# Kernel optimization log

Measured on AMD Instinct MI355X. Metric: run time of the kernel, lower is better.

Reference implementation:

```python
import jax, jax.numpy as jnp
import numpy as np

N, E = 50000, 800000
IN, HID, OUT = 128, 128, 64
H, ED = 4, 3
D = HID // H  # per-head dim = 32


def _w(key, shape):
    fan_in = shape[-1]
    return jax.random.normal(key, shape, dtype=jnp.float32) / np.sqrt(fan_in)


def setup_inputs() -> dict:
    key = jax.random.key(0)
    ks = jax.random.split(key, 32)
    inp = {
        "x": jax.random.normal(ks[0], (N, IN), dtype=jnp.float32),
        "edge_index": jax.random.randint(ks[1], (2, E), 0, N, dtype=jnp.int32),
        "edge_attr": jax.random.normal(ks[2], (E, ED), dtype=jnp.float32),
        # layer 1 TransformerConv (bias=False)
        "Wq1": _w(ks[3], (HID, IN)), "Wk1": _w(ks[4], (HID, IN)),
        "Wv1": _w(ks[5], (HID, IN)), "We1": _w(ks[6], (HID, ED)),
        "Ws1": _w(ks[7], (HID, IN)),
        # layer 1 MLP [HID,HID,HID]
        "M1a": _w(ks[8], (HID, HID)), "b1a": jnp.zeros((HID,), jnp.float32),
        "M1b": _w(ks[9], (HID, HID)), "b1b": jnp.zeros((HID,), jnp.float32),
        # layer 2 TransformerConv
        "Wq2": _w(ks[10], (HID, HID)), "Wk2": _w(ks[11], (HID, HID)),
        "Wv2": _w(ks[12], (HID, HID)), "We2": _w(ks[13], (HID, ED)),
        "Ws2": _w(ks[14], (HID, HID)),
        # layer 2 MLP
        "M2a": _w(ks[15], (HID, HID)), "b2a": jnp.zeros((HID,), jnp.float32),
        "M2b": _w(ks[16], (HID, HID)), "b2b": jnp.zeros((HID,), jnp.float32),
        # final MLP [HID,HID,OUT], plain_last=False
        "Wf1": _w(ks[17], (HID, HID)), "bf1": jnp.zeros((HID,), jnp.float32),
        "Wf2": _w(ks[18], (OUT, HID)), "bf2": jnp.zeros((OUT,), jnp.float32),
    }
    return inp


def _gelu(x):
    return jax.nn.gelu(x, approximate=True)


def _transformer_conv(x, src, dst, edge_attr, Wq, Wk, Wv, We, Ws, n_nodes):
    # PyG TransformerConv: x_j = x[src] (message source), x_i = x[dst] (target)
    q = (x @ Wq.T).reshape(n_nodes, H, D)
    e = (edge_attr @ We.T).reshape(-1, H, D)              # [E,H,D]
    k = (x @ Wk.T).reshape(n_nodes, H, D)[src] + e        # [E,H,D]
    v = (x @ Wv.T).reshape(n_nodes, H, D)[src] + e        # [E,H,D]
    alpha = jnp.einsum("ehd,ehd->eh", q[dst], k) / jnp.float32(np.sqrt(D))
    # segment softmax over incoming edges of each target node
    m = jax.ops.segment_max(alpha, dst, num_segments=n_nodes)  # [N,H]
    m = jnp.where(jnp.isfinite(m), m, 0.0)
    p = jnp.exp(alpha - m[dst])
    s = jax.ops.segment_sum(p, dst, num_segments=n_nodes)      # [N,H]
    a = p / jnp.maximum(s[dst], 1e-16)                         # [E,H]
    out = jax.ops.segment_sum(a[:, :, None] * v, dst, num_segments=n_nodes)
    out = out.reshape(n_nodes, H * D)
    # root_weight=True (default): skip connection through lin_skip (no bias)
    return out + x @ Ws.T


def _mlp2(x, Wa, ba, Wb, bb):
    # PyG MLP with plain_last=False: act after every linear, norm=None
    h = _gelu(x @ Wa.T + ba)
    return _gelu(h @ Wb.T + bb)


def reference(x, edge_index, edge_attr,
              Wq1, Wk1, Wv1, We1, Ws1, M1a, b1a, M1b, b1b,
              Wq2, Wk2, Wv2, We2, Ws2, M2a, b2a, M2b, b2b,
              Wf1, bf1, Wf2, bf2):
    n_nodes = x.shape[0]
    src, dst = edge_index[0], edge_index[1]
    h = _transformer_conv(x, src, dst, edge_attr, Wq1, Wk1, Wv1, We1, Ws1, n_nodes)
    h = h + _mlp2(h, M1a, b1a, M1b, b1b)
    h = _transformer_conv(h, src, dst, edge_attr, Wq2, Wk2, Wv2, We2, Ws2, n_nodes)
    h = h + _mlp2(h, M2a, b2a, M2b, b2b)
    return _mlp2(h, Wf1, bf1, Wf2, bf2)
```

## Files before the change

### kernel.cpp

```cpp
#include <hip/hip_runtime.h>
#include <hip/hip_bf16.h>
#include <math.h>

#define NN 50000
#define NE 800000
#define NPAD 50048
#define NB_SCAN 196

typedef unsigned short u16;
typedef unsigned int u32;
typedef __attribute__((ext_vector_type(8))) short short8;
typedef __attribute__((ext_vector_type(4))) float float4v;

__device__ __forceinline__ float us2f(u16 u) { return __uint_as_float(((unsigned)u) << 16); }
__device__ __forceinline__ float blo(u32 u) { return __uint_as_float(u << 16); }
__device__ __forceinline__ float bhi(u32 u) { return __uint_as_float(u & 0xffff0000u); }
__device__ __forceinline__ u16 f2us(float f) {
    unsigned x = __float_as_uint(f);
    return (u16)((x + 0x7FFFu + ((x >> 16) & 1u)) >> 16);
}
__device__ __forceinline__ float gelu_f(float x) {
    float p = x * x;
    float t = x * fmaf(p, 0.0713548162726f, 1.5957691216057308f);
    float e = __expf(-t);
    return x * __builtin_amdgcn_rcpf(1.0f + e);
}
__device__ __forceinline__ void lds_fence() {
    asm volatile("s_waitcnt lgkmcnt(0)" ::: "memory");
}

__device__ __forceinline__ float4v mfma4p(const u16* __restrict__ WP, int tile, int l,
                                          short8 a0, short8 a1, short8 a2, short8 a3) {
    const short8* wp = (const short8*)WP + (size_t)tile * 256 + l;
    short8 b0 = wp[0], b1 = wp[64], b2 = wp[128], b3 = wp[192];
    float4v acc = {0.f, 0.f, 0.f, 0.f};
    acc = __builtin_amdgcn_mfma_f32_16x16x32_bf16(a0, b0, acc, 0, 0, 0);
    acc = __builtin_amdgcn_mfma_f32_16x16x32_bf16(a1, b1, acc, 0, 0, 0);
    acc = __builtin_amdgcn_mfma_f32_16x16x32_bf16(a2, b2, acc, 0, 0, 0);
    acc = __builtin_amdgcn_mfma_f32_16x16x32_bf16(a3, b3, acc, 0, 0, 0);
    return acc;
}


__global__ void k_hist(const int* __restrict__ dstv, int* __restrict__ deg) {
    int e = blockIdx.x * blockDim.x + threadIdx.x;
    if (e < NE) atomicAdd(&deg[dstv[e]], 1);
}

__global__ __launch_bounds__(256) void k_scan1(const int* __restrict__ deg,
                                               int* __restrict__ rowstart,
                                               int* __restrict__ bsum) {
    __shared__ int wtot[4];
    int i = blockIdx.x * 256 + threadIdx.x;
    int lane = threadIdx.x & 63, w = threadIdx.x >> 6;
    int v = (i < NN) ? deg[i] : 0;
    int incl = v;
#pragma unroll
    for (int d = 1; d < 64; d <<= 1) {
        int tv = __shfl_up(incl, d);
        if (lane >= d) incl += tv;
    }
    if (lane == 63) wtot[w] = incl;
    __syncthreads();
    if (threadIdx.x == 0) {
        int s = 0;
#pragma unroll
        for (int j = 0; j < 4; ++j) { int t = wtot[j]; wtot[j] = s; s += t; }
        bsum[blockIdx.x] = s;
    }
    __syncthreads();
    if (i < NN) rowstart[i] = incl - v + wtot[w];
}

__global__ __launch_bounds__(256) void k_scan2(int* __restrict__ bsum) {
    __shared__ int wtot[4];
    int t = threadIdx.x;
    int lane = t & 63, w = t >> 6;
    int v = (t < NB_SCAN) ? bsum[t] : 0;
    int incl = v;
#pragma unroll
    for (int d = 1; d < 64; d <<= 1) {
        int tv = __shfl_up(incl, d);
        if (lane >= d) incl += tv;
    }
    if (lane == 63) wtot[w] = incl;
    __syncthreads();
    if (t == 0) {
        int s = 0;
#pragma unroll
        for (int j = 0; j < 4; ++j) { int tt = wtot[j]; wtot[j] = s; s += tt; }
    }
    __syncthreads();
    if (t < NB_SCAN) bsum[t] = incl - v + wtot[w];
}

__global__ void k_scan3(const int* __restrict__ bsum, int* __restrict__ rowstart,
                        int* __restrict__ cursor) {
    int i = blockIdx.x * 256 + threadIdx.x;
    if (i < NN) {
        int v = rowstart[i] + bsum[blockIdx.x];
        rowstart[i] = v;
        cursor[i] = v;
    }
    if (i == 0) rowstart[NN] = NE;
}

__global__ void k_scatter(const int* __restrict__ srcv, const int* __restrict__ dstv,
                          const float* __restrict__ eattr, int* __restrict__ cursor,
                          int4* __restrict__ rec) {
    int e = blockIdx.x * blockDim.x + threadIdx.x;
    if (e >= NE) return;
    int dst = dstv[e];
    int pos = atomicAdd(&cursor[dst], 1);
    int4 r;
    r.x = srcv[e];
    r.y = __float_as_int(eattr[e * 3 + 0]);
    r.z = __float_as_int(eattr[e * 3 + 1]);
    r.w = __float_as_int(eattr[e * 3 + 2]);
    rec[pos] = r;
}


struct CvtEnt { const float* s; u16* d; int n; float sc; };
struct CvtTab { CvtEnt e[14]; };
__global__ void k_cvt_w(CvtTab tab) {
    CvtEnt E = tab.e[blockIdx.x >> 3];
    int chunk = blockIdx.x & 7;
    int per = E.n >> 3;
    int lo = chunk * per, hi = lo + per;
    for (int o = lo + threadIdx.x; o < hi; o += blockDim.x) {
        int tile = o >> 11;
        int q = (o >> 9) & 3;
        int l = (o >> 3) & 63;
        int j = o & 7;
        int row = tile * 16 + (l & 15);
        int col = q * 32 + (l >> 4) * 8 + j;
        E.d[o] = f2us(E.s[row * 128 + col] * E.sc);
    }
}


__device__ __forceinline__ void stage_plain(u16* buf, int kb, int m, int tt, float4v acc) {
#pragma unroll
    for (int r = 0; r < 4; ++r) buf[(kb * 4 + r) * 136 + tt * 16 + m] = f2us(acc[r]);
}
__device__ __forceinline__ void store128(const u16* buf, u16* dst, int r0w, int coff, int l) {
#pragma unroll
    for (int it = 0; it < 4; ++it) {
        int j = it * 64 + l;
        int row = j >> 4, col = (j & 15) * 8;
        *(uint4*)(dst + (size_t)(r0w + row) * 512 + coff + col) = *(const uint4*)&buf[row * 136 + col];
    }
}
__device__ __forceinline__ void read_frags(const u16* buf, int m, int kb,
                                           short8& f0, short8& f1, short8& f2, short8& f3) {
    const u16* p = buf + m * 136 + kb * 8;
    f0 = *(const short8*)(p);
    f1 = *(const short8*)(p + 32);
    f2 = *(const short8*)(p + 64);
    f3 = *(const short8*)(p + 96);
}


__global__ __launch_bounds__(256, 4) void k_qkvs1(const float* __restrict__ Ain,
                                                  const u16* __restrict__ W,
                                                  u16* __restrict__ QKVS) {
    __shared__ u16 tile[4][16 * 136];
    int tid = threadIdx.x;
    int l = tid & 63, w = tid >> 6, m = l & 15, kb = l >> 4;
    int r0w = blockIdx.x * 64 + w * 16;
    u16* my = tile[w];

    short8 a0, a1, a2, a3;
    {
        const float* ap = Ain + (size_t)(r0w + m) * 128;
        bool ok = (r0w + m) < NN;
        short8* dsts[4] = {&a0, &a1, &a2, &a3};
#pragma unroll
        for (int i = 0; i < 4; ++i) {
            short8 r;
            if (ok) {
                const float* p = ap + (kb + i * 4) * 8;
                float4 f0 = *(const float4*)p;
                float4 f1 = *(const float4*)(p + 4);
                r[0]=(short)f2us(f0.x); r[1]=(short)f2us(f0.y); r[2]=(short)f2us(f0.z); r[3]=(short)f2us(f0.w);
                r[4]=(short)f2us(f1.x); r[5]=(short)f2us(f1.y); r[6]=(short)f2us(f1.z); r[7]=(short)f2us(f1.w);
            } else {
#pragma unroll
                for (int j = 0; j < 8; ++j) r[j] = 0;
            }
            *dsts[i] = r;
        }
    }

#pragma unroll
    for (int tt = 0; tt < 8; ++tt) stage_plain(my, kb, m, tt, mfma4p(W, tt, l, a0, a1, a2, a3));
    lds_fence();
    store128(my, QKVS, r0w, 0, l);
    lds_fence();
#pragma unroll
    for (int tt = 0; tt < 4; ++tt) {
        float4v acc = mfma4p(W, 8 + tt, l, a0, a1, a2, a3);
        int c = tt * 32 + 8 * (m >> 2) + (m & 3);
#pragma unroll
        for (int r = 0; r < 4; ++r) my[(kb * 4 + r) * 136 + c] = f2us(acc[r]);
    }
#pragma unroll
    for (int tt = 0; tt < 4; ++tt) {
        float4v acc = mfma4p(W, 16 + tt, l, a0, a1, a2, a3);
        int c = tt * 32 + 8 * (m >> 2) + (m & 3) + 4;
#pragma unroll
        for (int r = 0; r < 4; ++r) my[(kb * 4 + r) * 136 + c] = f2us(acc[r]);
    }
    lds_fence();
    store128(my, QKVS, r0w, 128, l);
    lds_fence();
#pragma unroll
    for (int tt = 0; tt < 4; ++tt) {
        float4v acc = mfma4p(W, 12 + tt, l, a0, a1, a2, a3);
        int c = tt * 32 + 8 * (m >> 2) + (m & 3);
#pragma unroll
        for (int r = 0; r < 4; ++r) my[(kb * 4 + r) * 136 + c] = f2us(acc[r]);
    }
#pragma unroll
    for (int tt = 0; tt < 4; ++tt) {
        float4v acc = mfma4p(W, 20 + tt, l, a0, a1, a2, a3);
        int c = tt * 32 + 8 * (m >> 2) + (m & 3) + 4;
#pragma unroll
        for (int r = 0; r < 4; ++r) my[(kb * 4 + r) * 136 + c] = f2us(acc[r]);
    }
    lds_fence();
    store128(my, QKVS, r0w, 256, l);
    lds_fence();
#pragma unroll
    for (int tt = 0; tt < 8; ++tt) stage_plain(my, kb, m, tt, mfma4p(W, 24 + tt, l, a0, a1, a2, a3));
    lds_fence();
    store128(my, QKVS, r0w, 384, l);
}


__global__ __launch_bounds__(256, 4) void k_mlp_qkvs(const u16* __restrict__ Ain,
                                                     const u16* __restrict__ Wm,
                                                     const float* __restrict__ bias1,
                                                     const float* __restrict__ bias2,
                                                     const u16* __restrict__ Wq,
                                                     u16* __restrict__ QKVS) {
    __shared__ u16 shb[4][16 * 136];
    __shared__ u16 t1b[4][16 * 136];
    int tid = threadIdx.x;
    int l = tid & 63, w = tid >> 6, m = l & 15, kb = l >> 4;
    int r0w = blockIdx.x * 64 + w * 16;
    u16* sh = shb[w];
    u16* t1 = t1b[w];

    const short8* arow = (const short8*)(Ain + (size_t)(r0w + m) * 128);
    short8 a0 = arow[kb], a1 = arow[kb + 4], a2 = arow[kb + 8], a3 = arow[kb + 12];
    {
        u16* p = sh + m * 136 + kb * 8;
        *(short8*)(p) = a0;
        *(short8*)(p + 32) = a1;
        *(short8*)(p + 64) = a2;
        *(short8*)(p + 96) = a3;
    }
#pragma unroll
    for (int tt = 0; tt < 8; ++tt) {
        float4v acc = mfma4p(Wm, tt, l, a0, a1, a2, a3);
        float bv = bias1[tt * 16 + m];
#pragma unroll
        for (int r = 0; r < 4; ++r)
            t1[(kb * 4 + r) * 136 + tt * 16 + m] = f2us(gelu_f(acc[r] + bv));
    }
    lds_fence();
    short8 c0, c1, c2, c3;
    read_frags(t1, m, kb, c0, c1, c2, c3);
#pragma unroll
    for (int tt = 0; tt < 8; ++tt) {
        float4v acc = mfma4p(Wm + 16384, tt, l, c0, c1, c2, c3);
        float bv = bias2[tt * 16 + m];
#pragma unroll
        for (int r = 0; r < 4; ++r) {
            int idx = (kb * 4 + r) * 136 + tt * 16 + m;
            sh[idx] = f2us(gelu_f(acc[r] + bv) + us2f(sh[idx]));
        }
    }
    lds_fence();
    short8 h0, h1, h2, h3;
    read_frags(sh, m, kb, h0, h1, h2, h3);

#pragma unroll
    for (int tt = 0; tt < 8; ++tt) stage_plain(t1, kb, m, tt, mfma4p(Wq, tt, l, h0, h1, h2, h3));
    lds_fence();
    store128(t1, QKVS, r0w, 0, l);
    lds_fence();
#pragma unroll
    for (int tt = 0; tt < 4; ++tt) {
        float4v acc = mfma4p(Wq, 8 + tt, l, h0, h1, h2, h3);
        int c = tt * 32 + 8 * (m >> 2) + (m & 3);
#pragma unroll
        for (int r = 0; r < 4; ++r) t1[(kb * 4 + r) * 136 + c] = f2us(acc[r]);
    }
#pragma unroll
    for (int tt = 0; tt < 4; ++tt) {
        float4v acc = mfma4p(Wq, 16 + tt, l, h0, h1, h2, h3);
        int c = tt * 32 + 8 * (m >> 2) + (m & 3) + 4;
#pragma unroll
        for (int r = 0; r < 4; ++r) t1[(kb * 4 + r) * 136 + c] = f2us(acc[r]);
    }
    lds_fence();
    store128(t1, QKVS, r0w, 128, l);
    lds_fence();
#pragma unroll
    for (int tt = 0; tt < 4; ++tt) {
        float4v acc = mfma4p(Wq, 12 + tt, l, h0, h1, h2, h3);
        int c = tt * 32 + 8 * (m >> 2) + (m & 3);
#pragma unroll
        for (int r = 0; r < 4; ++r) t1[(kb * 4 + r) * 136 + c] = f2us(acc[r]);
    }
#pragma unroll
    for (int tt = 0; tt < 4; ++tt) {
        float4v acc = mfma4p(Wq, 20 + tt, l, h0, h1, h2, h3);
        int c = tt * 32 + 8 * (m >> 2) + (m & 3) + 4;
#pragma unroll
        for (int r = 0; r < 4; ++r) t1[(kb * 4 + r) * 136 + c] = f2us(acc[r]);
    }
    lds_fence();
    store128(t1, QKVS, r0w, 256, l);
    lds_fence();
#pragma unroll
    for (int tt = 0; tt < 8; ++tt) stage_plain(t1, kb, m, tt, mfma4p(Wq, 24 + tt, l, h0, h1, h2, h3));
    lds_fence();
    store128(t1, QKVS, r0w, 384, l);
}


__global__ __launch_bounds__(256, 4) void k_mlp_final(const u16* __restrict__ Ain,
                                                      const u16* __restrict__ Wm,
                                                      const float* __restrict__ bias1,
                                                      const float* __restrict__ bias2,
                                                      const u16* __restrict__ Wf,
                                                      const float* __restrict__ bf1,
                                                      const float* __restrict__ bf2,
                                                      float* __restrict__ outp) {
    __shared__ u16 shb[4][16 * 136];
    __shared__ u16 t1b[4][16 * 136];
    int tid = threadIdx.x;
    int l = tid & 63, w = tid >> 6, m = l & 15, kb = l >> 4;
    int r0w = blockIdx.x * 64 + w * 16;
    u16* sh = shb[w];
    u16* t1 = t1b[w];

    const short8* arow = (const short8*)(Ain + (size_t)(r0w + m) * 128);
    short8 a0 = arow[kb], a1 = arow[kb + 4], a2 = arow[kb + 8], a3 = arow[kb + 12];
    {
        u16* p = sh + m * 136 + kb * 8;
        *(short8*)(p) = a0;
        *(short8*)(p + 32) = a1;
        *(short8*)(p + 64) = a2;
        *(short8*)(p + 96) = a3;
    }
#pragma unroll
    for (int tt = 0; tt < 8; ++tt) {
        float4v acc = mfma4p(Wm, tt, l, a0, a1, a2, a3);
        float bv = bias1[tt * 16 + m];
#pragma unroll
        for (int r = 0; r < 4; ++r)
            t1[(kb * 4 + r) * 136 + tt * 16 + m] = f2us(gelu_f(acc[r] + bv));
    }
    lds_fence();
    short8 c0, c1, c2, c3;
    read_frags(t1, m, kb, c0, c1, c2, c3);
#pragma unroll
    for (int tt = 0; tt < 8; ++tt) {
        float4v acc = mfma4p(Wm + 16384, tt, l, c0, c1, c2, c3);
        float bv = bias2[tt * 16 + m];
#pragma unroll
        for (int r = 0; r < 4; ++r) {
            int idx = (kb * 4 + r) * 136 + tt * 16 + m;
            sh[idx] = f2us(gelu_f(acc[r] + bv) + us2f(sh[idx]));
        }
    }
    lds_fence();
    short8 h0, h1, h2, h3;
    read_frags(sh, m, kb, h0, h1, h2, h3);
#pragma unroll
    for (int tt = 0; tt < 8; ++tt) {
        float4v acc = mfma4p(Wf, tt, l, h0, h1, h2, h3);
        float bv = bf1[tt * 16 + m];
#pragma unroll
        for (int r = 0; r < 4; ++r)
            t1[(kb * 4 + r) * 136 + tt * 16 + m] = f2us(gelu_f(acc[r] + bv));
    }
    lds_fence();
    short8 f0, f1, f2, f3;
    read_frags(t1, m, kb, f0, f1, f2, f3);
    lds_fence();
#pragma unroll
    for (int tt = 0; tt < 4; ++tt) {
        float4v acc = mfma4p(Wf + 16384, tt, l, f0, f1, f2, f3);
        float bv = bf2[tt * 16 + m];
#pragma unroll
        for (int r = 0; r < 4; ++r)
            t1[(kb * 4 + r) * 136 + tt * 16 + m] = f2us(gelu_f(acc[r] + bv));
    }
    lds_fence();
#pragma unroll
    for (int it = 0; it < 2; ++it) {
        int j = it * 64 + l;
        int row = j >> 3, col = (j & 7) * 8;
        int grow = r0w + row;
        if (grow < NN) {
            uint4 pk = *(const uint4*)&t1[row * 136 + col];
            const u16* pv = (const u16*)&pk;
            float* po = outp + (size_t)grow * 64 + col;
            float4 o0 = {us2f(pv[0]), us2f(pv[1]), us2f(pv[2]), us2f(pv[3])};
            float4 o1 = {us2f(pv[4]), us2f(pv[5]), us2f(pv[6]), us2f(pv[7])};
            *(float4*)po = o0;
            *(float4*)(po + 4) = o1;
        }
    }
}


__global__ __launch_bounds__(256, 6) void k_conv(const int* __restrict__ rowstart,
                                                 const int4* __restrict__ rec,
                                                 const u16* __restrict__ qkvs,
                                                 const float* __restrict__ We,
                                                 u16* __restrict__ out) {
    int n = blockIdx.x * 4 + (threadIdx.x >> 6);
    int l = threadIdx.x & 63;
    int half = l >> 5;
    int li = l & 31;
    int c0 = (li >> 3) * 32 + (li & 7) * 4;
    const u16* qrow = qkvs + (size_t)n * 512;
    uint2 qu = *(const uint2*)(qrow + c0);
    uint2 su = *(const uint2*)(qrow + 384 + c0);
    float q0 = blo(qu.x), q1 = bhi(qu.x), q2 = blo(qu.y), q3 = bhi(qu.y);
    float g0, g1, g2;
    {
        const float* wp = We + c0 * 3;
        g0 = fmaf(q3, wp[9],  fmaf(q2, wp[6], fmaf(q1, wp[3], q0 * wp[0])));
        g1 = fmaf(q3, wp[10], fmaf(q2, wp[7], fmaf(q1, wp[4], q0 * wp[1])));
        g2 = fmaf(q3, wp[11], fmaf(q2, wp[8], fmaf(q1, wp[5], q0 * wp[2])));
#pragma unroll
        for (int d = 1; d <= 4; d <<= 1) {
            g0 += __shfl_xor(g0, d);
            g1 += __shfl_xor(g1, d);
            g2 += __shfl_xor(g2, d);
        }
    }
    int e0 = rowstart[n], e1 = rowstart[n + 1];
    int cnt = e1 - e0;
    float ss = 0.f, o0 = 0.f, o1 = 0.f, o2 = 0.f, o3 = 0.f, S0 = 0.f, S1 = 0.f, S2 = 0.f;
    int kvoff = 128 + li * 8;

    auto edge = [&](int4 r, uint4 kv) {
        float part = fmaf(q3, bhi(kv.y), fmaf(q2, blo(kv.y), fmaf(q1, bhi(kv.x), q0 * blo(kv.x))));
        part += __shfl_xor(part, 1);
        part += __shfl_xor(part, 2);
        part += __shfl_xor(part, 4);
        float ea0 = __int_as_float(r.y), ea1 = __int_as_float(r.z), ea2 = __int_as_float(r.w);
        float alpha = fmaf(ea2, g2, fmaf(ea1, g1, fmaf(ea0, g0, part)));
        float p = __expf(fminf(alpha, 80.f));
        o0 = fmaf(p, blo(kv.z), o0);
        o1 = fmaf(p, bhi(kv.z), o1);
        o2 = fmaf(p, blo(kv.w), o2);
        o3 = fmaf(p, bhi(kv.w), o3);
        ss += p;
        S0 = fmaf(p, ea0, S0);
        S1 = fmaf(p, ea1, S1);
        S2 = fmaf(p, ea2, S2);
    };

    int Kh = (cnt - half + 1) >> 1;
    int e = e0 + half;
    int k = 0;
    for (; k + 4 <= Kh; k += 4, e += 8) {
        int4 r0 = rec[e], r1 = rec[e + 2], r2 = rec[e + 4], r3 = rec[e + 6];
        uint4 k0 = *(const uint4*)(qkvs + (u32)(r0.x * 512 + kvoff));
        uint4 k1 = *(const uint4*)(qkvs + (u32)(r1.x * 512 + kvoff));
        uint4 k2 = *(const uint4*)(qkvs + (u32)(r2.x * 512 + kvoff));
        uint4 k3 = *(const uint4*)(qkvs + (u32)(r3.x * 512 + kvoff));
        edge(r0, k0);
        edge(r1, k1);
        edge(r2, k2);
        edge(r3, k3);
    }
    if (k + 2 <= Kh) {
        int4 r0 = rec[e], r1 = rec[e + 2];
        uint4 k0 = *(const uint4*)(qkvs + (u32)(r0.x * 512 + kvoff));
        uint4 k1 = *(const uint4*)(qkvs + (u32)(r1.x * 512 + kvoff));
        edge(r0, k0);
        edge(r1, k1);
        k += 2;
        e += 4;
    }
    if (k < Kh) {
        int4 r0 = rec[e];
        uint4 k0 = *(const uint4*)(qkvs + (u32)(r0.x * 512 + kvoff));
        edge(r0, k0);
    }

    o0 += __shfl_xor(o0, 32);
    o1 += __shfl_xor(o1, 32);
    o2 += __shfl_xor(o2, 32);
    o3 += __shfl_xor(o3, 32);
    ss += __shfl_xor(ss, 32);
    S0 += __shfl_xor(S0, 32);
    S1 += __shfl_xor(S1, 32);
    S2 += __shfl_xor(S2, 32);
    if (half == 0) {
        float inv = __builtin_amdgcn_rcpf(fmaxf(ss, 1e-16f));
        const float* wp = We + c0 * 3;
        o0 = fmaf(wp[2],  S2, fmaf(wp[1],  S1, fmaf(wp[0], S0, o0)));
        o1 = fmaf(wp[5],  S2, fmaf(wp[4],  S1, fmaf(wp[3], S0, o1)));
        o2 = fmaf(wp[8],  S2, fmaf(wp[7],  S1, fmaf(wp[6], S0, o2)));
        o3 = fmaf(wp[11], S2, fmaf(wp[10], S1, fmaf(wp[9], S0, o3)));
        float r0v = fmaf(o0, inv, blo(su.x));
        float r1v = fmaf(o1, inv, bhi(su.x));
        float r2v = fmaf(o2, inv, blo(su.y));
        float r3v = fmaf(o3, inv, bhi(su.y));
        uint2 ou;
        ou.x = (u32)f2us(r0v) | ((u32)f2us(r1v) << 16);
        ou.y = (u32)f2us(r2v) | ((u32)f2us(r3v) << 16);
        *(uint2*)(out + (size_t)n * 128 + c0) = ou;
    }
}


extern "C" void kernel_launch(void* const* d_in, const int* in_sizes, int n_in,
                              void* d_out, int out_size, void* d_ws, size_t ws_size,
                              hipStream_t stream) {
    const float* x = (const float*)d_in[0];
    const int* ei = (const int*)d_in[1];
    const float* eattr = (const float*)d_in[2];
    const float* Wq1 = (const float*)d_in[3];
    const float* Wk1 = (const float*)d_in[4];
    const float* Wv1 = (const float*)d_in[5];
    const float* We1 = (const float*)d_in[6];
    const float* Ws1 = (const float*)d_in[7];
    const float* M1a = (const float*)d_in[8];
    const float* b1a = (const float*)d_in[9];
    const float* M1b = (const float*)d_in[10];
    const float* b1b = (const float*)d_in[11];
    const float* Wq2 = (const float*)d_in[12];
    const float* Wk2 = (const float*)d_in[13];
    const float* Wv2 = (const float*)d_in[14];
    const float* We2 = (const float*)d_in[15];
    const float* Ws2 = (const float*)d_in[16];
    const float* M2a = (const float*)d_in[17];
    const float* b2a = (const float*)d_in[18];
    const float* M2b = (const float*)d_in[19];
    const float* b2b = (const float*)d_in[20];
    const float* Wf1 = (const float*)d_in[21];
    const float* bf1 = (const float*)d_in[22];
    const float* Wf2 = (const float*)d_in[23];
    const float* bf2 = (const float*)d_in[24];

    char* ws = (char*)d_ws;
    size_t off = 0;
    auto alloc = [&](size_t bytes) -> void* {
        void* p = ws + off;
        off = (off + bytes + 255) & ~(size_t)255;
        return p;
    };
    int* deg = (int*)alloc((size_t)NN * 4);
    int* rowstart = (int*)alloc((size_t)(NN + 1) * 4);
    int* cursor = (int*)alloc((size_t)NN * 4);
    int* bsum = (int*)alloc((size_t)NB_SCAN * 4);
    int4* rec = (int4*)alloc((size_t)NE * 16);
    u16* QKVS = (u16*)alloc((size_t)NPAD * 512 * 2);
    u16* Ha = (u16*)alloc((size_t)NPAD * 128 * 2);
    u16* WB[14];
    const int wsz[14] = {16384, 16384, 16384, 16384, 16384, 16384, 16384,
                         16384, 16384, 16384, 16384, 16384, 16384, 8192};
    for (int i = 0; i < 14; ++i) WB[i] = (u16*)alloc((size_t)wsz[i] * 2);

    const int* srcv = ei;
    const int* dstv = ei + NE;

    hipMemsetAsync(deg, 0, (size_t)NN * 4, stream);
    k_hist<<<(NE + 255) / 256, 256, 0, stream>>>(dstv, deg);
    k_scan1<<<NB_SCAN, 256, 0, stream>>>(deg, rowstart, bsum);
    k_scan2<<<1, 256, 0, stream>>>(bsum);
    k_scan3<<<NB_SCAN, 256, 0, stream>>>(bsum, rowstart, cursor);
    k_scatter<<<(NE + 255) / 256, 256, 0, stream>>>(srcv, dstv, eattr, cursor, rec);

    CvtTab tab;
    const float* wsrc[14] = {Wq1, Wk1, Wv1, Ws1, Wq2, Wk2, Wv2, Ws2,
                             M1a, M1b, M2a, M2b, Wf1, Wf2};
    const float SC = 0.17677669529663687f;
    for (int i = 0; i < 14; ++i) {
        tab.e[i].s = wsrc[i];
        tab.e[i].d = WB[i];
        tab.e[i].n = wsz[i];
        tab.e[i].sc = (i == 0 || i == 4) ? SC : 1.0f;
    }
    k_cvt_w<<<112, 256, 0, stream>>>(tab);

    dim3 blk(256);
    dim3 grd(NPAD / 64);
    dim3 gconv(NN / 4);

    k_qkvs1<<<grd, blk, 0, stream>>>(x, WB[0], QKVS);
    k_conv<<<gconv, blk, 0, stream>>>(rowstart, rec, QKVS, We1, Ha);
    k_mlp_qkvs<<<grd, blk, 0, stream>>>(Ha, WB[8], b1a, b1b, WB[4], QKVS);
    k_conv<<<gconv, blk, 0, stream>>>(rowstart, rec, QKVS, We2, Ha);
    k_mlp_final<<<grd, blk, 0, stream>>>(Ha, WB[10], b2a, b2b, WB[12], bf1, bf2, (float*)d_out);
}
```

Measured before the change: 407.8 us.

## Quantize gathered K/V to int8 with per-row-head scales for edge conv

Result: no change. 406.4 us (-0.3%).

```diff
diff --git a/kernel.cpp b/kernel.cpp
--- a/kernel.cpp
+++ b/kernel.cpp
@@ -9,6 +9,7 @@
 
 typedef unsigned short u16;
 typedef unsigned int u32;
+typedef unsigned char u8;
 typedef __attribute__((ext_vector_type(8))) short short8;
 typedef __attribute__((ext_vector_type(4))) float float4v;
 
@@ -28,6 +29,20 @@
 __device__ __forceinline__ void lds_fence() {
     asm volatile("s_waitcnt lgkmcnt(0)" ::: "memory");
 }
+
+#if __has_builtin(__builtin_amdgcn_sdot4)
+__device__ __forceinline__ int dot4i8(int a, int b) {
+    return __builtin_amdgcn_sdot4(a, b, 0, false);
+}
+#else
+__device__ __forceinline__ int dot4i8(int a, int b) {
+    int r = ((a << 24) >> 24) * ((b << 24) >> 24);
+    r += ((a << 16) >> 24) * ((b << 16) >> 24);
+    r += ((a << 8) >> 24) * ((b << 8) >> 24);
+    r += (a >> 24) * (b >> 24);
+    return r;
+}
+#endif
 
 __device__ __forceinline__ float4v mfma4p(const u16* __restrict__ WP, int tile, int l,
                                           short8 a0, short8 a1, short8 a2, short8 a3) {
@@ -144,12 +159,49 @@
 #pragma unroll
     for (int r = 0; r < 4; ++r) buf[(kb * 4 + r) * 136 + tt * 16 + m] = f2us(acc[r]);
 }
-__device__ __forceinline__ void store128(const u16* buf, u16* dst, int r0w, int coff, int l) {
+__device__ __forceinline__ void store_qs(const u16* buf, u16* dst, int r0w, int coff, int l) {
 #pragma unroll
     for (int it = 0; it < 4; ++it) {
         int j = it * 64 + l;
         int row = j >> 4, col = (j & 15) * 8;
-        *(uint4*)(dst + (size_t)(r0w + row) * 512 + coff + col) = *(const uint4*)&buf[row * 136 + col];
+        *(uint4*)(dst + (size_t)(r0w + row) * 256 + coff + col) = *(const uint4*)&buf[row * 136 + col];
+    }
+}
+__device__ __forceinline__ void kv_scales(const u16* buf, float* sclw, float* __restrict__ SCL,
+                                          int r0w, int halfsel, int l) {
+    int rr = l & 15;
+    int hl = (l >> 4) & 1;
+    int kind = l >> 5;
+    const u16* base = buf + rr * 136 + hl * 64 + kind * 4;
+    unsigned mx = 0;
+#pragma unroll
+    for (int p = 0; p < 8; ++p) {
+        uint2 w = *(const uint2*)(base + p * 8);
+        unsigned a = w.x & 0x7fff7fffu, b = w.y & 0x7fff7fffu;
+        unsigned m1 = max(a & 0xffffu, a >> 16);
+        unsigned m2 = max(b & 0xffffu, b >> 16);
+        mx = max(mx, max(m1, m2));
+    }
+    float ma = fmaxf(us2f((u16)mx), 1e-20f);
+    float inv = 127.0f * __builtin_amdgcn_rcpf(ma);
+    sclw[rr * 4 + kind * 2 + hl] = inv;
+    SCL[(size_t)(r0w + rr) * 8 + (hl + halfsel * 2) * 2 + kind] = ma * (1.0f / 127.0f);
+}
+__device__ __forceinline__ void kv_to_i8(const u16* buf, const float* sclw,
+                                         u8* __restrict__ kvq, int r0w, int halfoff, int l) {
+    int ch = l & 31;
+    int rsel = l >> 5;
+#pragma unroll
+    for (int it = 0; it < 8; ++it) {
+        int rr = it * 2 + rsel;
+        uint2 w = *(const uint2*)&buf[rr * 136 + ch * 4];
+        float inv = sclw[rr * 4 + (ch & 1) * 2 + (ch >> 4)];
+        int i0 = __float2int_rn(blo(w.x) * inv);
+        int i1 = __float2int_rn(bhi(w.x) * inv);
+        int i2 = __float2int_rn(blo(w.y) * inv);
+        int i3 = __float2int_rn(bhi(w.y) * inv);
+        unsigned pk = (i0 & 255) | ((i1 & 255) << 8) | ((i2 & 255) << 16) | ((unsigned)(i3 & 255) << 24);
+        *(unsigned*)(kvq + (size_t)(r0w + rr) * 256 + halfoff + ch * 4) = pk;
     }
 }
 __device__ __forceinline__ void read_frags(const u16* buf, int m, int kb,
@@ -164,12 +216,16 @@
 
 __global__ __launch_bounds__(256, 4) void k_qkvs1(const float* __restrict__ Ain,
                                                   const u16* __restrict__ W,
-                                                  u16* __restrict__ QKVS) {
+                                                  u16* __restrict__ QS,
+                                                  u8* __restrict__ KVQ,
+                                                  float* __restrict__ SCL) {
     __shared__ u16 tile[4][16 * 136];
+    __shared__ float scl[4][64];
     int tid = threadIdx.x;
     int l = tid & 63, w = tid >> 6, m = l & 15, kb = l >> 4;
     int r0w = blockIdx.x * 64 + w * 16;
     u16* my = tile[w];
+    float* sw = scl[w];
 
     short8 a0, a1, a2, a3;
     {
@@ -196,7 +252,7 @@
 #pragma unroll
     for (int tt = 0; tt < 8; ++tt) stage_plain(my, kb, m, tt, mfma4p(W, tt, l, a0, a1, a2, a3));
     lds_fence();
-    store128(my, QKVS, r0w, 0, l);
+    store_qs(my, QS, r0w, 0, l);
     lds_fence();
 #pragma unroll
     for (int tt = 0; tt < 4; ++tt) {
@@ -213,7 +269,9 @@
         for (int r = 0; r < 4; ++r) my[(kb * 4 + r) * 136 + c] = f2us(acc[r]);
     }
     lds_fence();
-    store128(my, QKVS, r0w, 128, l);
+    kv_scales(my, sw, SCL, r0w, 0, l);
+    lds_fence();
+    kv_to_i8(my, sw, KVQ, r0w, 0, l);
     lds_fence();
 #pragma unroll
     for (int tt = 0; tt < 4; ++tt) {
@@ -230,12 +288,14 @@
         for (int r = 0; r < 4; ++r) my[(kb * 4 + r) * 136 + c] = f2us(acc[r]);
     }
     lds_fence();
-    store128(my, QKVS, r0w, 256, l);
+    kv_scales(my, sw, SCL, r0w, 1, l);
+    lds_fence();
+    kv_to_i8(my, sw, KVQ, r0w, 128, l);
     lds_fence();
 #pragma unroll
     for (int tt = 0; tt < 8; ++tt) stage_plain(my, kb, m, tt, mfma4p(W, 24 + tt, l, a0, a1, a2, a3));
     lds_fence();
-    store128(my, QKVS, r0w, 384, l);
+    store_qs(my, QS, r0w, 128, l);
 }
 
 
@@ -244,14 +304,18 @@
                                                      const float* __restrict__ bias1,
                                                      const float* __restrict__ bias2,
                                                      const u16* __restrict__ Wq,
-                                                     u16* __restrict__ QKVS) {
+                                                     u16* __restrict__ QS,
+                                                     u8* __restrict__ KVQ,
+                                                     float* __restrict__ SCL) {
     __shared__ u16 shb[4][16 * 136];
     __shared__ u16 t1b[4][16 * 136];
+    __shared__ float scl[4][64];
     int tid = threadIdx.x;
     int l = tid & 63, w = tid >> 6, m = l & 15, kb = l >> 4;
     int r0w = blockIdx.x * 64 + w * 16;
     u16* sh = shb[w];
     u16* t1 = t1b[w];
+    float* sw = scl[w];
 
     const short8* arow = (const short8*)(Ain + (size_t)(r0w + m) * 128);
     short8 a0 = arow[kb], a1 = arow[kb + 4], a2 = arow[kb + 8], a3 = arow[kb + 12];
@@ -290,7 +354,7 @@
 #pragma unroll
     for (int tt = 0; tt < 8; ++tt) stage_plain(t1, kb, m, tt, mfma4p(Wq, tt, l, h0, h1, h2, h3));
     lds_fence();
-    store128(t1, QKVS, r0w, 0, l);
+    store_qs(t1, QS, r0w, 0, l);
     lds_fence();
 #pragma unroll
     for (int tt = 0; tt < 4; ++tt) {
@@ -307,7 +371,9 @@
         for (int r = 0; r < 4; ++r) t1[(kb * 4 + r) * 136 + c] = f2us(acc[r]);
     }
     lds_fence();
-    store128(t1, QKVS, r0w, 128, l);
+    kv_scales(t1, sw, SCL, r0w, 0, l);
+    lds_fence();
+    kv_to_i8(t1, sw, KVQ, r0w, 0, l);
     lds_fence();
 #pragma unroll
     for (int tt = 0; tt < 4; ++tt) {
@@ -324,12 +390,14 @@
         for (int r = 0; r < 4; ++r) t1[(kb * 4 + r) * 136 + c] = f2us(acc[r]);
     }
     lds_fence();
-    store128(t1, QKVS, r0w, 256, l);
+    kv_scales(t1, sw, SCL, r0w, 1, l);
+    lds_fence();
+    kv_to_i8(t1, sw, KVQ, r0w, 128, l);
     lds_fence();
 #pragma unroll
     for (int tt = 0; tt < 8; ++tt) stage_plain(t1, kb, m, tt, mfma4p(Wq, 24 + tt, l, h0, h1, h2, h3));
     lds_fence();
-    store128(t1, QKVS, r0w, 384, l);
+    store_qs(t1, QS, r0w, 128, l);
 }
 
 
@@ -423,7 +491,9 @@
 
 __global__ __launch_bounds__(256, 6) void k_conv(const int* __restrict__ rowstart,
                                                  const int4* __restrict__ rec,
-                                                 const u16* __restrict__ qkvs,
+                                                 const u16* __restrict__ QS,
+                                                 const u8* __restrict__ KVQ,
+                                                 const float* __restrict__ SCL,
                                                  const float* __restrict__ We,
                                                  u16* __restrict__ out) {
     int n = blockIdx.x * 4 + (threadIdx.x >> 6);
@@ -431,9 +501,9 @@
     int half = l >> 5;
     int li = l & 31;
     int c0 = (li >> 3) * 32 + (li & 7) * 4;
-    const u16* qrow = qkvs + (size_t)n * 512;
+    const u16* qrow = QS + (size_t)n * 256;
     uint2 qu = *(const uint2*)(qrow + c0);
-    uint2 su = *(const uint2*)(qrow + 384 + c0);
+    uint2 su = *(const uint2*)(qrow + 128 + c0);
     float q0 = blo(qu.x), q1 = bhi(qu.x), q2 = blo(qu.y), q3 = bhi(qu.y);
     float g0, g1, g2;
     {
@@ -448,23 +518,42 @@
             g2 += __shfl_xor(g2, d);
         }
     }
+    float aq = fmaxf(fmaxf(fabsf(q0), fabsf(q1)), fmaxf(fabsf(q2), fabsf(q3)));
+    aq = fmaxf(aq, __shfl_xor(aq, 1));
+    aq = fmaxf(aq, __shfl_xor(aq, 2));
+    aq = fmaxf(aq, __shfl_xor(aq, 4));
+    aq = fmaxf(aq, 1e-20f);
+    float qiv = 127.0f * __builtin_amdgcn_rcpf(aq);
+    int j0 = __float2int_rn(q0 * qiv), j1 = __float2int_rn(q1 * qiv);
+    int j2 = __float2int_rn(q2 * qiv), j3 = __float2int_rn(q3 * qiv);
+    int q8 = (j0 & 255) | ((j1 & 255) << 8) | ((j2 & 255) << 16) | ((j3 & 255) << 24);
+    float qsc = aq * (1.0f / 127.0f);
+
     int e0 = rowstart[n], e1 = rowstart[n + 1];
     int cnt = e1 - e0;
     float ss = 0.f, o0 = 0.f, o1 = 0.f, o2 = 0.f, o3 = 0.f, S0 = 0.f, S1 = 0.f, S2 = 0.f;
-    int kvoff = 128 + li * 8;
-
-    auto edge = [&](int4 r, uint4 kv) {
-        float part = fmaf(q3, bhi(kv.y), fmaf(q2, blo(kv.y), fmaf(q1, bhi(kv.x), q0 * blo(kv.x))));
-        part += __shfl_xor(part, 1);
-        part += __shfl_xor(part, 2);
-        part += __shfl_xor(part, 4);
+    const u8* kvb = KVQ + li * 8;
+    const float* sclb = SCL + (li >> 3) * 2;
+
+    auto edge = [&](int4 r, uint2 kv, float2 sc) {
+        int pi = dot4i8(q8, (int)kv.x);
+        pi += __shfl_xor(pi, 1);
+        pi += __shfl_xor(pi, 2);
+        pi += __shfl_xor(pi, 4);
         float ea0 = __int_as_float(r.y), ea1 = __int_as_float(r.z), ea2 = __int_as_float(r.w);
-        float alpha = fmaf(ea2, g2, fmaf(ea1, g1, fmaf(ea0, g0, part)));
+        float base = fmaf(ea2, g2, fmaf(ea1, g1, ea0 * g0));
+        float alpha = fmaf((float)pi, qsc * sc.x, base);
         float p = __expf(fminf(alpha, 80.f));
-        o0 = fmaf(p, blo(kv.z), o0);
-        o1 = fmaf(p, bhi(kv.z), o1);
-        o2 = fmaf(p, blo(kv.w), o2);
-        o3 = fmaf(p, bhi(kv.w), o3);
+        float pv = p * sc.y;
+        int vv = (int)kv.y;
+        float v0 = (float)((vv << 24) >> 24);
+        float v1 = (float)((vv << 16) >> 24);
+        float v2 = (float)((vv << 8) >> 24);
+        float v3 = (float)(vv >> 24);
+        o0 = fmaf(pv, v0, o0);
+        o1 = fmaf(pv, v1, o1);
+        o2 = fmaf(pv, v2, o2);
+        o3 = fmaf(pv, v3, o3);
         ss += p;
         S0 = fmaf(p, ea0, S0);
         S1 = fmaf(p, ea1, S1);
@@ -476,28 +565,35 @@
     int k = 0;
     for (; k + 4 <= Kh; k += 4, e += 8) {
         int4 r0 = rec[e], r1 = rec[e + 2], r2 = rec[e + 4], r3 = rec[e + 6];
-        uint4 k0 = *(const uint4*)(qkvs + (u32)(r0.x * 512 + kvoff));
-        uint4 k1 = *(const uint4*)(qkvs + (u32)(r1.x * 512 + kvoff));
-        uint4 k2 = *(const uint4*)(qkvs + (u32)(r2.x * 512 + kvoff));
-        uint4 k3 = *(const uint4*)(qkvs + (u32)(r3.x * 512 + kvoff));
-        edge(r0, k0);
-        edge(r1, k1);
-        edge(r2, k2);
-        edge(r3, k3);
+        uint2 k0 = *(const uint2*)(kvb + (u32)(r0.x * 256));
+        uint2 k1 = *(const uint2*)(kvb + (u32)(r1.x * 256));
+        uint2 k2 = *(const uint2*)(kvb + (u32)(r2.x * 256));
+        uint2 k3 = *(const uint2*)(kvb + (u32)(r3.x * 256));
+        float2 s0 = *(const float2*)(sclb + (u32)(r0.x * 8));
+        float2 s1 = *(const float2*)(sclb + (u32)(r1.x * 8));
+        float2 s2 = *(const float2*)(sclb + (u32)(r2.x * 8));
+        float2 s3 = *(const float2*)(sclb + (u32)(r3.x * 8));
+        edge(r0, k0, s0);
+        edge(r1, k1, s1);
+        edge(r2, k2, s2);
+        edge(r3, k3, s3);
     }
     if (k + 2 <= Kh) {
         int4 r0 = rec[e], r1 = rec[e + 2];
-        uint4 k0 = *(const uint4*)(qkvs + (u32)(r0.x * 512 + kvoff));
-        uint4 k1 = *(const uint4*)(qkvs + (u32)(r1.x * 512 + kvoff));
-        edge(r0, k0);
-        edge(r1, k1);
+        uint2 k0 = *(const uint2*)(kvb + (u32)(r0.x * 256));
+        uint2 k1 = *(const uint2*)(kvb + (u32)(r1.x * 256));
+        float2 s0 = *(const float2*)(sclb + (u32)(r0.x * 8));
+        float2 s1 = *(const float2*)(sclb + (u32)(r1.x * 8));
+        edge(r0, k0, s0);
+        edge(r1, k1, s1);
         k += 2;
         e += 4;
     }
     if (k < Kh) {
         int4 r0 = rec[e];
-        uint4 k0 = *(const uint4*)(qkvs + (u32)(r0.x * 512 + kvoff));
-        edge(r0, k0);
+        uint2 k0 = *(const uint2*)(kvb + (u32)(r0.x * 256));
+        float2 s0 = *(const float2*)(sclb + (u32)(r0.x * 8));
+        edge(r0, k0, s0);
     }
 
     o0 += __shfl_xor(o0, 32);
@@ -568,7 +664,9 @@
     int* cursor = (int*)alloc((size_t)NN * 4);
     int* bsum = (int*)alloc((size_t)NB_SCAN * 4);
     int4* rec = (int4*)alloc((size_t)NE * 16);
-    u16* QKVS = (u16*)alloc((size_t)NPAD * 512 * 2);
+    u16* QS = (u16*)alloc((size_t)NPAD * 256 * 2);
+    u8* KVQ = (u8*)alloc((size_t)NPAD * 256);
+    float* SCL = (float*)alloc((size_t)NPAD * 32);
     u16* Ha = (u16*)alloc((size_t)NPAD * 128 * 2);
     u16* WB[14];
     const int wsz[14] = {16384, 16384, 16384, 16384, 16384, 16384, 16384,
@@ -601,9 +699,9 @@
     dim3 grd(NPAD / 64);
     dim3 gconv(NN / 4);
 
-    k_qkvs1<<<grd, blk, 0, stream>>>(x, WB[0], QKVS);
-    k_conv<<<gconv, blk, 0, stream>>>(rowstart, rec, QKVS, We1, Ha);
-    k_mlp_qkvs<<<grd, blk, 0, stream>>>(Ha, WB[8], b1a, b1b, WB[4], QKVS);
-    k_conv<<<gconv, blk, 0, stream>>>(rowstart, rec, QKVS, We2, Ha);
+    k_qkvs1<<<grd, blk, 0, stream>>>(x, WB[0], QS, KVQ, SCL);
+    k_conv<<<gconv, blk, 0, stream>>>(rowstart, rec, QS, KVQ, SCL, We1, Ha);
+    k_mlp_qkvs<<<grd, blk, 0, stream>>>(Ha, WB[8], b1a, b1b, WB[4], QS, KVQ, SCL);
+    k_conv<<<gconv, blk, 0, stream>>>(rowstart, rec, QS, KVQ, SCL, We2, Ha);
     k_mlp_final<<<grd, blk, 0, stream>>>(Ha, WB[10], b2a, b2b, WB[12], bf1, bf2, (float*)d_out);
 }
```
